# Performance work log

Hardware: AMD Instinct MI355X
Metric: run time of the kernel (lower is better)

The kernel has to match this reference:

```python
import jax, jax.numpy as jnp
import numpy as np

B, N, M, D, H = 2, 4096, 4096, 512, 8
P = D // H


def setup_inputs() -> dict:
    key = jax.random.key(0)
    ks = jax.random.split(key, 9)
    s = 1.0 / np.sqrt(D)
    return {
        "queries": jax.random.normal(ks[0], (B, N, D), dtype=jnp.float32),
        "keys": jax.random.normal(ks[1], (B, M, D), dtype=jnp.float32),
        "values": jax.random.normal(ks[2], (B, M, D), dtype=jnp.float32),
        "Wq": jax.random.normal(ks[3], (D, D), dtype=jnp.float32) * s,
        "bq": jax.random.normal(ks[4], (D,), dtype=jnp.float32) * s,
        "Wk": jax.random.normal(ks[5], (D, D), dtype=jnp.float32) * s,
        "bk": jax.random.normal(ks[6], (D,), dtype=jnp.float32) * s,
        "Wv": jax.random.normal(ks[7], (D, D), dtype=jnp.float32) * s,
        "bv": jax.random.normal(ks[8], (D,), dtype=jnp.float32) * s,
    }


def reference(queries, keys, values, Wq, bq, Wk, bk, Wv, bv):
    b, n, d = queries.shape
    m = keys.shape[1]
    h, p = H, D // H
    temperature = jnp.asarray(p, queries.dtype) ** 0.5
    # Linear projections (torch Linear: x @ W^T + b; here W stored as [in, out])
    q = (queries @ Wq + bq).reshape(b, n, h, p)
    k = (keys @ Wk + bk).reshape(b, m, h, p)
    v = (values @ Wv + bv).reshape(b, m, h, p)
    # scaled dot-product attention per head; scores [b, h, n, m]
    scores = jnp.einsum("bnhp,bmhp->bhnm", q, k) / temperature
    attn = jax.nn.softmax(scores, axis=-1)
    out = jnp.einsum("bhnm,bmhp->bnhp", attn, v)
    return out.reshape(b, n, d)
```

## Files before the change

kernel.cpp:

```cpp
#include <hip/hip_runtime.h>
#include <stdint.h>

#define B_ 2
#define N_ 4096
#define M_ 4096
#define D_ 512
#define H_ 8
#define P_ 64

typedef short bf16x8 __attribute__((ext_vector_type(8)));
typedef float f32x4 __attribute__((ext_vector_type(4)));
typedef unsigned short u16;
typedef unsigned int u32;
typedef u32 u32x4 __attribute__((ext_vector_type(4)));

static __device__ __forceinline__ u16 f2bf(float f) {
  u32 u = __builtin_bit_cast(u32, f);
  u32 r = u + 0x7fffu + ((u >> 16) & 1u);
  return (u16)(r >> 16);
}

static __device__ __forceinline__ u32 cvtpk(float lo, float hi_) {
  u32 d;
  asm("v_cvt_pk_bf16_f32 %0, %1, %2" : "=v"(d) : "v"(lo), "v"(hi_));
  return d;
}

static __device__ __forceinline__ float fexp2(float x) {
  float r;
  asm("v_exp_f32 %0, %1" : "=v"(r) : "v"(x));
  return r;
}

static __device__ __forceinline__ u32 permpk(const bf16x8& a0, const bf16x8& a1, int i) {
  u32x4 a0w = __builtin_bit_cast(u32x4, a0);
  u32x4 a1w = __builtin_bit_cast(u32x4, a1);
  int wd = i >> 1;
  u32 sel = (i & 1) ? 0x07060302u : 0x05040100u;
  return __builtin_amdgcn_perm(a1w[wd], a0w[wd], sel);
}

__global__ __launch_bounds__(256) void wt_kernel(const float* __restrict__ Wq,
                                                 const float* __restrict__ Wk,
                                                 const float* __restrict__ Wv,
                                                 u16* __restrict__ Wt) {
  __shared__ float tile[32][33];
  int z = blockIdx.z;
  const float* W = (z == 0) ? Wq : (z == 1) ? Wk : Wv;
  u16* out = Wt + (size_t)z * D_ * D_;
  int o0 = blockIdx.x * 32, d0 = blockIdx.y * 32;
  int tx = threadIdx.x, ty = threadIdx.y;
#pragma unroll
  for (int k = 0; k < 4; k++) tile[ty + k * 8][tx] = W[(size_t)(d0 + ty + k * 8) * D_ + o0 + tx];
  __syncthreads();
#pragma unroll
  for (int k = 0; k < 4; k++) out[(size_t)(o0 + ty + k * 8) * D_ + d0 + tx] = f2bf(tile[tx][ty + k * 8]);
}

__global__ __launch_bounds__(256) void proj_kernel(const float* __restrict__ Xq,
                                                   const float* __restrict__ Xk,
                                                   const float* __restrict__ Xv,
                                                   const u16* __restrict__ Wt,
                                                   const float* __restrict__ bq,
                                                   const float* __restrict__ bk,
                                                   const float* __restrict__ bv,
                                                   u16* __restrict__ QKV) {
  int bid = blockIdx.x;
  int xcd = bid & 7, idx = bid >> 3;
  int xb = idx & 3, gg = idx >> 2;
  int yz = xcd + 8 * gg;
  int yb = yz & 63, z = yz >> 6;

  const float* X = (z == 0) ? Xq : (z == 1) ? Xk : Xv;
  const float* bias = (z == 0) ? bq : (z == 1) ? bk : bv;
  const u16* W = Wt + (size_t)z * D_ * D_;
  u16* Y = QKV + (size_t)z * (B_ * N_ * D_);
  const float scale = (z == 0) ? 0.18033688011112042f : 1.0f;

  __shared__ u16 Alds[2][128 * 32];
  __shared__ u16 Blds[2][128 * 32];
  char* AL = (char*)&Alds[0][0];
  char* BL = (char*)&Blds[0][0];

  int t = threadIdx.x;
  int lane = t & 63, w = t >> 6;
  int wm = w >> 1, wn = w & 1;
  int l15 = lane & 15, g = lane >> 4;
  int rb = yb * 128, ob = xb * 128;

  int awoff = (t >> 3) * 64 + (((t & 7) * 8) ^ (((t >> 3) & 3) << 4));
  int bwoff = (t >> 2) * 64 + (((t & 3) * 16) ^ (((t >> 2) & 3) << 4));
  const float* xg = X + (size_t)(rb + (t >> 3)) * D_ + (t & 7) * 4;
  const u16* wg = W + (size_t)(ob + (t >> 2)) * D_ + (t & 3) * 8;

  int aroff = (wm * 64 + l15) * 64 + ((g * 16) ^ ((l15 & 3) << 4));
  int broff = (wn * 64 + l15) * 64 + ((g * 16) ^ ((l15 & 3) << 4));

  const f32x4 zero4 = {0.f, 0.f, 0.f, 0.f};
  f32x4 acc[4][4];
#pragma unroll
  for (int m = 0; m < 4; m++)
#pragma unroll
    for (int n = 0; n < 4; n++) acc[m][n] = zero4;

  {
#pragma unroll
    for (int i = 0; i < 4; i++) {
      float4 v = *(const float4*)(xg + (size_t)(32 * i) * D_);
      uint2 d;
      d.x = cvtpk(v.x, v.y);
      d.y = cvtpk(v.z, v.w);
      *(uint2*)(AL + awoff + i * 2048) = d;
    }
#pragma unroll
    for (int i = 0; i < 2; i++)
      *(bf16x8*)(BL + bwoff + i * 4096) = *(const bf16x8*)(wg + (size_t)(64 * i) * D_);
  }
  awoff ^= 0x2000;
  bwoff ^= 0x2000;
  __syncthreads();

  for (int kt = 0; kt < 16; kt++) {
    float4 ax0 = {}, ax1 = {}, ax2 = {}, ax3 = {};
    bf16x8 bx0 = {}, bx1 = {};
    if (kt < 15) {
      const float* xp = xg + (kt + 1) * 32;
      const u16* wp = wg + (kt + 1) * 32;
      ax0 = *(const float4*)(xp);
      ax1 = *(const float4*)(xp + (size_t)32 * D_);
      ax2 = *(const float4*)(xp + (size_t)64 * D_);
      ax3 = *(const float4*)(xp + (size_t)96 * D_);
      bx0 = *(const bf16x8*)(wp);
      bx1 = *(const bf16x8*)(wp + (size_t)64 * D_);
    }

    bf16x8 a[4], b[4];
#pragma unroll
    for (int m = 0; m < 4; m++) a[m] = *(const bf16x8*)(AL + aroff + m * 1024);
#pragma unroll
    for (int n = 0; n < 4; n++) b[n] = *(const bf16x8*)(BL + broff + n * 1024);
#pragma unroll
    for (int m = 0; m < 4; m++)
#pragma unroll
      for (int n = 0; n < 4; n++)
        acc[m][n] = __builtin_amdgcn_mfma_f32_16x16x32_bf16(a[m], b[n], acc[m][n], 0, 0, 0);

    if (kt < 15) {
      uint2 d;
      d.x = cvtpk(ax0.x, ax0.y);
      d.y = cvtpk(ax0.z, ax0.w);
      *(uint2*)(AL + awoff) = d;
      d.x = cvtpk(ax1.x, ax1.y);
      d.y = cvtpk(ax1.z, ax1.w);
      *(uint2*)(AL + awoff + 2048) = d;
      d.x = cvtpk(ax2.x, ax2.y);
      d.y = cvtpk(ax2.z, ax2.w);
      *(uint2*)(AL + awoff + 4096) = d;
      d.x = cvtpk(ax3.x, ax3.y);
      d.y = cvtpk(ax3.z, ax3.w);
      *(uint2*)(AL + awoff + 6144) = d;
      *(bf16x8*)(BL + bwoff) = bx0;
      *(bf16x8*)(BL + bwoff + 4096) = bx1;
    }
    awoff ^= 0x2000;
    bwoff ^= 0x2000;
    aroff ^= 0x2000;
    broff ^= 0x2000;
    __syncthreads();
  }

#pragma unroll
  for (int n = 0; n < 4; n++) {
    int col = ob + wn * 64 + n * 16 + l15;
    float bv_ = bias[col];
#pragma unroll
    for (int m = 0; m < 4; m++) {
      int row0 = rb + wm * 64 + m * 16 + g * 4;
#pragma unroll
      for (int r = 0; r < 4; r++) {
        float y = (acc[m][n][r] + bv_) * scale;
        Y[(size_t)(row0 + r) * D_ + col] = f2bf(y);
      }
    }
  }
}

__global__ __launch_bounds__(512, 2) void attn_kernel(const u16* __restrict__ QKV,
                                                      float* __restrict__ out) {
  const u16* Q = QKV;
  const u16* K = QKV + (size_t)(B_ * N_ * D_);
  const u16* V = K + (size_t)(B_ * N_ * D_);

  __shared__ u16 Klds[2][128 * 64];
  __shared__ u16 Vlds[2][2][64 * 64];

  char* KL = (char*)&Klds[0][0];
  char* VL = (char*)&Vlds[0][0][0];

  int t = threadIdx.x, l = t & 63, w = t >> 6;
  int l15 = l & 15, g = (l >> 4) & 3;
  int swz = (l15 & 7) << 4;

  int bid = blockIdx.x + 16 * (blockIdx.y + 8 * blockIdx.z);
  int sbid = (bid & 7) * 32 + (bid >> 3);
  int qt = sbid & 15, h = (sbid >> 4) & 7, b = sbid >> 7;
  int qwa = qt * 256 + w * 16;
  int qwb = qwa + 128;

  const u16* Kb = K + (size_t)(b * M_) * D_ + h * P_;
  const u16* Vb = V + (size_t)(b * M_) * D_ + h * P_;

  bf16x8 qfa[2], qfb[2];
  const u16* qrow_a = Q + (size_t)(b * N_ + qwa + l15) * D_ + h * P_;
  const u16* qrow_b = Q + (size_t)(b * N_ + qwb + l15) * D_ + h * P_;
#pragma unroll
  for (int step = 0; step < 2; step++) {
    qfa[step] = *(const bf16x8*)(qrow_a + step * 32 + g * 8);
    qfb[step] = *(const bf16x8*)(qrow_b + step * 32 + g * 8);
  }

  int koff0 = l15 * 128 + ((g * 16) ^ swz);
  int koff1 = l15 * 128 + ((64 + g * 16) ^ swz);
  int voff0 = koff0, voff1 = koff1;

  int krow = t >> 3, kc = t & 7;
  int kwoff = krow * 128 + ((kc * 16) ^ ((krow & 7) << 4));
  const u16* kg0 = Kb + (size_t)krow * D_ + kc * 8;
  const u16* kg1 = kg0 + (size_t)64 * D_;
  int hv = t >> 8, th = t & 255;
  int kp = th & 31, p0 = (th >> 5) * 8;
  int kv0 = 2 * kp, blk2 = kv0 >> 5, ww_ = kv0 & 31;
  int slot = blk2 * 32 + ((ww_ >> 2) & 3) * 8 + ((ww_ >> 4) << 2) + (ww_ & 3);
  int vwB = hv * 0x2000 + p0 * 128 + 2 * slot;
  const u16* vg0 = Vb + (size_t)(hv * 64 + kv0) * D_ + p0;
  const u16* vg1 = vg0 + D_;

  const f32x4 zc = {0.f, 0.f, 0.f, 0.f};
  const u32x4 onesw = {0x3F803F80u, 0x3F803F80u, 0x3F803F80u, 0x3F803F80u};
  const bf16x8 ones_f = __builtin_bit_cast(bf16x8, onesw);
  f32x4 oa[4], ob_[4], ol_a = zc, ol_b = zc;
#pragma unroll
  for (int i = 0; i < 4; i++) {
    oa[i] = zc;
    ob_[i] = zc;
  }

  {
    *(bf16x8*)(KL + kwoff) = *(const bf16x8*)kg0;
    *(bf16x8*)(KL + kwoff + 8192) = *(const bf16x8*)kg1;
    bf16x8 a0 = *(const bf16x8*)vg0;
    bf16x8 a1 = *(const bf16x8*)vg1;
#pragma unroll
    for (int i = 0; i < 8; i++) *(u32*)(VL + ((vwB ^ (i << 4)) + i * 128)) = permpk(a0, a1, i);
  }
  kwoff ^= 0x4000;
  vwB ^= 0x4000;
  const u16* kgp0 = kg0 + (size_t)128 * D_;
  const u16* kgp1 = kg1 + (size_t)128 * D_;
  const u16* vgp0 = vg0 + (size_t)128 * D_;
  const u16* vgp1 = vg1 + (size_t)128 * D_;
  __syncthreads();

  const int NT = M_ / 128;
  for (int kt = 0; kt < NT; kt++) {
    bf16x8 kn0 = {}, kn1 = {}, vn0 = {}, vn1 = {};
    if (kt + 1 < NT) {
      kn0 = *(const bf16x8*)kgp0;
      kn1 = *(const bf16x8*)kgp1;
      vn0 = *(const bf16x8*)vgp0;
      vn1 = *(const bf16x8*)vgp1;
      kgp0 += (size_t)128 * D_;
      kgp1 += (size_t)128 * D_;
      vgp0 += (size_t)128 * D_;
      vgp1 += (size_t)128 * D_;
    }

    f32x4 sa0[4], sb0[4], sa1[4], sb1[4];

    __builtin_amdgcn_s_setprio(1);
#pragma unroll
    for (int tt = 0; tt < 4; tt++) {
      bf16x8 kf0 = *(const bf16x8*)(KL + koff0 + tt * 2048);
      sa0[tt] = __builtin_amdgcn_mfma_f32_16x16x32_bf16(kf0, qfa[0], zc, 0, 0, 0);
      sb0[tt] = __builtin_amdgcn_mfma_f32_16x16x32_bf16(kf0, qfb[0], zc, 0, 0, 0);
      bf16x8 kf1 = *(const bf16x8*)(KL + koff1 + tt * 2048);
      sa0[tt] = __builtin_amdgcn_mfma_f32_16x16x32_bf16(kf1, qfa[1], sa0[tt], 0, 0, 0);
      sb0[tt] = __builtin_amdgcn_mfma_f32_16x16x32_bf16(kf1, qfb[1], sb0[tt], 0, 0, 0);
    }
#pragma unroll
    for (int tt = 0; tt < 4; tt++) {
      bf16x8 kf0 = *(const bf16x8*)(KL + koff0 + 8192 + tt * 2048);
      sa1[tt] = __builtin_amdgcn_mfma_f32_16x16x32_bf16(kf0, qfa[0], zc, 0, 0, 0);
      sb1[tt] = __builtin_amdgcn_mfma_f32_16x16x32_bf16(kf0, qfb[0], zc, 0, 0, 0);
      bf16x8 kf1 = *(const bf16x8*)(KL + koff1 + 8192 + tt * 2048);
      sa1[tt] = __builtin_amdgcn_mfma_f32_16x16x32_bf16(kf1, qfa[1], sa1[tt], 0, 0, 0);
      sb1[tt] = __builtin_amdgcn_mfma_f32_16x16x32_bf16(kf1, qfb[1], sb1[tt], 0, 0, 0);
    }
    __builtin_amdgcn_s_setprio(0);

    u32 pwa0[2][4], pwb0[2][4];
#pragma unroll
    for (int tt = 0; tt < 4; tt++)
#pragma unroll
      for (int r = 0; r < 4; r++) {
        sa0[tt][r] = fexp2(sa0[tt][r]);
        sb0[tt][r] = fexp2(sb0[tt][r]);
      }
#pragma unroll
    for (int kb2 = 0; kb2 < 2; kb2++)
#pragma unroll
      for (int wd = 0; wd < 4; wd++) {
        const f32x4& sva = sa0[2 * kb2 + (wd >> 1)];
        const f32x4& svb = sb0[2 * kb2 + (wd >> 1)];
        pwa0[kb2][wd] = cvtpk(sva[(wd & 1) * 2], sva[(wd & 1) * 2 + 1]);
        pwb0[kb2][wd] = cvtpk(svb[(wd & 1) * 2], svb[(wd & 1) * 2 + 1]);
      }

    __builtin_amdgcn_s_setprio(1);
#pragma unroll
    for (int kb2 = 0; kb2 < 2; kb2++) {
      u32x4 pva = {pwa0[kb2][0], pwa0[kb2][1], pwa0[kb2][2], pwa0[kb2][3]};
      u32x4 pvb = {pwb0[kb2][0], pwb0[kb2][1], pwb0[kb2][2], pwb0[kb2][3]};
      bf16x8 pfa = __builtin_bit_cast(bf16x8, pva);
      bf16x8 pfb = __builtin_bit_cast(bf16x8, pvb);
      int voff = kb2 ? voff1 : voff0;
#pragma unroll
      for (int tt = 0; tt < 4; tt++) {
        bf16x8 vf = *(const bf16x8*)(VL + voff + tt * 2048);
        oa[tt] = __builtin_amdgcn_mfma_f32_16x16x32_bf16(vf, pfa, oa[tt], 0, 0, 0);
        ob_[tt] = __builtin_amdgcn_mfma_f32_16x16x32_bf16(vf, pfb, ob_[tt], 0, 0, 0);
      }
      ol_a = __builtin_amdgcn_mfma_f32_16x16x32_bf16(ones_f, pfa, ol_a, 0, 0, 0);
      ol_b = __builtin_amdgcn_mfma_f32_16x16x32_bf16(ones_f, pfb, ol_b, 0, 0, 0);
    }
    __builtin_amdgcn_s_setprio(0);

    u32 pwa1[2][4], pwb1[2][4];
#pragma unroll
    for (int tt = 0; tt < 4; tt++)
#pragma unroll
      for (int r = 0; r < 4; r++) {
        sa1[tt][r] = fexp2(sa1[tt][r]);
        sb1[tt][r] = fexp2(sb1[tt][r]);
      }
#pragma unroll
    for (int kb2 = 0; kb2 < 2; kb2++)
#pragma unroll
      for (int wd = 0; wd < 4; wd++) {
        const f32x4& sva = sa1[2 * kb2 + (wd >> 1)];
        const f32x4& svb = sb1[2 * kb2 + (wd >> 1)];
        pwa1[kb2][wd] = cvtpk(sva[(wd & 1) * 2], sva[(wd & 1) * 2 + 1]);
        pwb1[kb2][wd] = cvtpk(svb[(wd & 1) * 2], svb[(wd & 1) * 2 + 1]);
      }

    __builtin_amdgcn_s_setprio(1);
#pragma unroll
    for (int kb2 = 0; kb2 < 2; kb2++) {
      u32x4 pva = {pwa1[kb2][0], pwa1[kb2][1], pwa1[kb2][2], pwa1[kb2][3]};
      u32x4 pvb = {pwb1[kb2][0], pwb1[kb2][1], pwb1[kb2][2], pwb1[kb2][3]};
      bf16x8 pfa = __builtin_bit_cast(bf16x8, pva);
      bf16x8 pfb = __builtin_bit_cast(bf16x8, pvb);
      int voff = (kb2 ? voff1 : voff0) + 0x2000;
#pragma unroll
      for (int tt = 0; tt < 4; tt++) {
        bf16x8 vf = *(const bf16x8*)(VL + voff + tt * 2048);
        oa[tt] = __builtin_amdgcn_mfma_f32_16x16x32_bf16(vf, pfa, oa[tt], 0, 0, 0);
        ob_[tt] = __builtin_amdgcn_mfma_f32_16x16x32_bf16(vf, pfb, ob_[tt], 0, 0, 0);
      }
      ol_a = __builtin_amdgcn_mfma_f32_16x16x32_bf16(ones_f, pfa, ol_a, 0, 0, 0);
      ol_b = __builtin_amdgcn_mfma_f32_16x16x32_bf16(ones_f, pfb, ol_b, 0, 0, 0);
    }
    __builtin_amdgcn_s_setprio(0);

    if (kt + 1 < NT) {
      *(bf16x8*)(KL + kwoff) = kn0;
      *(bf16x8*)(KL + kwoff + 8192) = kn1;
#pragma unroll
      for (int i = 0; i < 8; i++) *(u32*)(VL + ((vwB ^ (i << 4)) + i * 128)) = permpk(vn0, vn1, i);
    }
    koff0 ^= 0x4000;
    koff1 ^= 0x4000;
    voff0 ^= 0x4000;
    voff1 ^= 0x4000;
    kwoff ^= 0x4000;
    vwB ^= 0x4000;
    __syncthreads();
  }

  float rla = 1.0f / ol_a[0], rlb = 1.0f / ol_b[0];
  float* orow_a = out + (size_t)(b * N_ + qwa + l15) * D_ + h * P_;
  float* orow_b = out + (size_t)(b * N_ + qwb + l15) * D_ + h * P_;
#pragma unroll
  for (int tt = 0; tt < 4; tt++) {
    float4 sta = {oa[tt][0] * rla, oa[tt][1] * rla, oa[tt][2] * rla, oa[tt][3] * rla};
    *(float4*)(orow_a + tt * 16 + g * 4) = sta;
    float4 stb = {ob_[tt][0] * rlb, ob_[tt][1] * rlb, ob_[tt][2] * rlb, ob_[tt][3] * rlb};
    *(float4*)(orow_b + tt * 16 + g * 4) = stb;
  }
}

extern "C" void kernel_launch(void* const* d_in, const int* in_sizes, int n_in,
                              void* d_out, int out_size, void* d_ws, size_t ws_size,
                              hipStream_t stream) {
  const float* queries = (const float*)d_in[0];
  const float* keys = (const float*)d_in[1];
  const float* values = (const float*)d_in[2];
  const float* Wq = (const float*)d_in[3];
  const float* bq = (const float*)d_in[4];
  const float* Wk = (const float*)d_in[5];
  const float* bk = (const float*)d_in[6];
  const float* Wv = (const float*)d_in[7];
  const float* bv = (const float*)d_in[8];
  float* out = (float*)d_out;

  u16* QKV = (u16*)d_ws;
  u16* Wt = QKV + (size_t)3 * B_ * N_ * D_;

  wt_kernel<<<dim3(16, 16, 3), dim3(32, 8), 0, stream>>>(Wq, Wk, Wv, Wt);
  proj_kernel<<<768, 256, 0, stream>>>(queries, keys, values, Wt, bq, bk, bv, QKV);
  attn_kernel<<<dim3(16, 8, 2), 512, 0, stream>>>(QKV, out);
}
```

Measured before the change: 107.4 us.

## Software-pipeline attention by deferring second-half softmax/PV across iterations

Restructures the attention main loop into a 4-way unrolled pipeline. The second half of each K tile's scores is carried into the next iteration, where its exp/convert/PV work overlaps the next tile's QK MFMAs. V staging is split into a double-buffered first half and a 4-deep ring for the deferred second half, with a drain step after the loop. The launch bound drops from two blocks per CU to one, freeing registers for the extra live score tiles at the cost of occupancy.

Result: faster. 105.3 us (-2.0%).

```diff
diff --git a/kernel.cpp b/kernel.cpp
--- a/kernel.cpp
+++ b/kernel.cpp
@@ -185,17 +185,164 @@
   }
 }
 
-__global__ __launch_bounds__(512, 2) void attn_kernel(const u16* __restrict__ QKV,
+struct AttnCtx {
+  const bf16x8* qfa;
+  const bf16x8* qfb;
+  f32x4 (*oa)[4];
+  f32x4 (*ob)[4];
+  f32x4* ol_a;
+  f32x4* ol_b;
+  char* KL;
+  char* V0L;
+  char* V1L;
+  int kro0, kro1, vro0, vro1, kwoff, vwloc, hv;
+  bf16x8 ones_f;
+};
+
+template <int U>
+static __device__ __forceinline__ void attn_pos(const AttnCtx& c, bool dodefer, bool dostage,
+                                                f32x4 (&cura)[4], f32x4 (&curb)[4],
+                                                f32x4 (&preva)[4], f32x4 (&prevb)[4],
+                                                const u16*& kgp0, const u16*& kgp1,
+                                                const u16*& vgp0, const u16*& vgp1) {
+  constexpr int KB = (U & 1) * 0x4000;
+  constexpr int V0B = (U & 1) * 0x2000;
+  constexpr int V1PREV = ((U + 3) & 3) * 0x2000;
+  constexpr int KBN = ((U + 1) & 1) * 0x4000;
+  constexpr int V0BN = ((U + 1) & 1) * 0x2000;
+  constexpr int V1BN = ((U + 1) & 3) * 0x2000;
+  const f32x4 zc = {0.f, 0.f, 0.f, 0.f};
+
+  bf16x8 kn0 = {}, kn1 = {}, vn0 = {}, vn1 = {};
+  if (dostage) {
+    kn0 = *(const bf16x8*)kgp0;
+    kn1 = *(const bf16x8*)kgp1;
+    vn0 = *(const bf16x8*)vgp0;
+    vn1 = *(const bf16x8*)vgp1;
+    kgp0 += (size_t)128 * D_;
+    kgp1 += (size_t)128 * D_;
+    vgp0 += (size_t)128 * D_;
+    vgp1 += (size_t)128 * D_;
+  }
+
+  f32x4 s0a[4], s0b[4];
+  __builtin_amdgcn_s_setprio(1);
+#pragma unroll
+  for (int tt = 0; tt < 4; tt++) {
+    bf16x8 kf0 = *(const bf16x8*)(c.KL + KB + c.kro0 + tt * 2048);
+    s0a[tt] = __builtin_amdgcn_mfma_f32_16x16x32_bf16(kf0, c.qfa[0], zc, 0, 0, 0);
+    s0b[tt] = __builtin_amdgcn_mfma_f32_16x16x32_bf16(kf0, c.qfb[0], zc, 0, 0, 0);
+    bf16x8 kf1 = *(const bf16x8*)(c.KL + KB + c.kro1 + tt * 2048);
+    s0a[tt] = __builtin_amdgcn_mfma_f32_16x16x32_bf16(kf1, c.qfa[1], s0a[tt], 0, 0, 0);
+    s0b[tt] = __builtin_amdgcn_mfma_f32_16x16x32_bf16(kf1, c.qfb[1], s0b[tt], 0, 0, 0);
+  }
+#pragma unroll
+  for (int tt = 0; tt < 4; tt++) {
+    bf16x8 kf0 = *(const bf16x8*)(c.KL + KB + 8192 + c.kro0 + tt * 2048);
+    cura[tt] = __builtin_amdgcn_mfma_f32_16x16x32_bf16(kf0, c.qfa[0], zc, 0, 0, 0);
+    curb[tt] = __builtin_amdgcn_mfma_f32_16x16x32_bf16(kf0, c.qfb[0], zc, 0, 0, 0);
+    bf16x8 kf1 = *(const bf16x8*)(c.KL + KB + 8192 + c.kro1 + tt * 2048);
+    cura[tt] = __builtin_amdgcn_mfma_f32_16x16x32_bf16(kf1, c.qfa[1], cura[tt], 0, 0, 0);
+    curb[tt] = __builtin_amdgcn_mfma_f32_16x16x32_bf16(kf1, c.qfb[1], curb[tt], 0, 0, 0);
+  }
+  __builtin_amdgcn_s_setprio(0);
+
+  if (dodefer) {
+    u32 pwa[2][4], pwb[2][4];
+#pragma unroll
+    for (int tt = 0; tt < 4; tt++)
+#pragma unroll
+      for (int r = 0; r < 4; r++) {
+        preva[tt][r] = fexp2(preva[tt][r]);
+        prevb[tt][r] = fexp2(prevb[tt][r]);
+      }
+#pragma unroll
+    for (int kb2 = 0; kb2 < 2; kb2++)
+#pragma unroll
+      for (int wd = 0; wd < 4; wd++) {
+        const f32x4& sva = preva[2 * kb2 + (wd >> 1)];
+        const f32x4& svb = prevb[2 * kb2 + (wd >> 1)];
+        pwa[kb2][wd] = cvtpk(sva[(wd & 1) * 2], sva[(wd & 1) * 2 + 1]);
+        pwb[kb2][wd] = cvtpk(svb[(wd & 1) * 2], svb[(wd & 1) * 2 + 1]);
+      }
+    __builtin_amdgcn_s_setprio(1);
+#pragma unroll
+    for (int kb2 = 0; kb2 < 2; kb2++) {
+      u32x4 pva = {pwa[kb2][0], pwa[kb2][1], pwa[kb2][2], pwa[kb2][3]};
+      u32x4 pvb = {pwb[kb2][0], pwb[kb2][1], pwb[kb2][2], pwb[kb2][3]};
+      bf16x8 pfa = __builtin_bit_cast(bf16x8, pva);
+      bf16x8 pfb = __builtin_bit_cast(bf16x8, pvb);
+      int voff = V1PREV + (kb2 ? c.vro1 : c.vro0);
+#pragma unroll
+      for (int tt = 0; tt < 4; tt++) {
+        bf16x8 vf = *(const bf16x8*)(c.V1L + voff + tt * 2048);
+        (*c.oa)[tt] = __builtin_amdgcn_mfma_f32_16x16x32_bf16(vf, pfa, (*c.oa)[tt], 0, 0, 0);
+        (*c.ob)[tt] = __builtin_amdgcn_mfma_f32_16x16x32_bf16(vf, pfb, (*c.ob)[tt], 0, 0, 0);
+      }
+      *c.ol_a = __builtin_amdgcn_mfma_f32_16x16x32_bf16(c.ones_f, pfa, *c.ol_a, 0, 0, 0);
+      *c.ol_b = __builtin_amdgcn_mfma_f32_16x16x32_bf16(c.ones_f, pfb, *c.ol_b, 0, 0, 0);
+    }
+    __builtin_amdgcn_s_setprio(0);
+  }
+
+  {
+    u32 pwa[2][4], pwb[2][4];
+#pragma unroll
+    for (int tt = 0; tt < 4; tt++)
+#pragma unroll
+      for (int r = 0; r < 4; r++) {
+        s0a[tt][r] = fexp2(s0a[tt][r]);
+        s0b[tt][r] = fexp2(s0b[tt][r]);
+      }
+#pragma unroll
+    for (int kb2 = 0; kb2 < 2; kb2++)
+#pragma unroll
+      for (int wd = 0; wd < 4; wd++) {
+        const f32x4& sva = s0a[2 * kb2 + (wd >> 1)];
+        const f32x4& svb = s0b[2 * kb2 + (wd >> 1)];
+        pwa[kb2][wd] = cvtpk(sva[(wd & 1) * 2], sva[(wd & 1) * 2 + 1]);
+        pwb[kb2][wd] = cvtpk(svb[(wd & 1) * 2], svb[(wd & 1) * 2 + 1]);
+      }
+    __builtin_amdgcn_s_setprio(1);
+#pragma unroll
+    for (int kb2 = 0; kb2 < 2; kb2++) {
+      u32x4 pva = {pwa[kb2][0], pwa[kb2][1], pwa[kb2][2], pwa[kb2][3]};
+      u32x4 pvb = {pwb[kb2][0], pwb[kb2][1], pwb[kb2][2], pwb[kb2][3]};
+      bf16x8 pfa = __builtin_bit_cast(bf16x8, pva);
+      bf16x8 pfb = __builtin_bit_cast(bf16x8, pvb);
+      int voff = V0B + (kb2 ? c.vro1 : c.vro0);
+#pragma unroll
+      for (int tt = 0; tt < 4; tt++) {
+        bf16x8 vf = *(const bf16x8*)(c.V0L + voff + tt * 2048);
+        (*c.oa)[tt] = __builtin_amdgcn_mfma_f32_16x16x32_bf16(vf, pfa, (*c.oa)[tt], 0, 0, 0);
+        (*c.ob)[tt] = __builtin_amdgcn_mfma_f32_16x16x32_bf16(vf, pfb, (*c.ob)[tt], 0, 0, 0);
+      }
+      *c.ol_a = __builtin_amdgcn_mfma_f32_16x16x32_bf16(c.ones_f, pfa, *c.ol_a, 0, 0, 0);
+      *c.ol_b = __builtin_amdgcn_mfma_f32_16x16x32_bf16(c.ones_f, pfb, *c.ol_b, 0, 0, 0);
+    }
+    __builtin_amdgcn_s_setprio(0);
+  }
+
+  if (dostage) {
+    *(bf16x8*)(c.KL + KBN + c.kwoff) = kn0;
+    *(bf16x8*)(c.KL + KBN + c.kwoff + 8192) = kn1;
+    char* vdst = c.hv ? (c.V1L + V1BN) : (c.V0L + V0BN);
+#pragma unroll
+    for (int i = 0; i < 8; i++)
+      *(u32*)(vdst + ((c.vwloc ^ (i << 4)) + i * 128)) = permpk(vn0, vn1, i);
+  }
+  __syncthreads();
+}
+
+__global__ __launch_bounds__(512, 1) void attn_kernel(const u16* __restrict__ QKV,
                                                       float* __restrict__ out) {
   const u16* Q = QKV;
   const u16* K = QKV + (size_t)(B_ * N_ * D_);
   const u16* V = K + (size_t)(B_ * N_ * D_);
 
   __shared__ u16 Klds[2][128 * 64];
-  __shared__ u16 Vlds[2][2][64 * 64];
-
-  char* KL = (char*)&Klds[0][0];
-  char* VL = (char*)&Vlds[0][0][0];
+  __shared__ u16 V0lds[2][64 * 64];
+  __shared__ u16 V1lds[4][64 * 64];
 
   int t = threadIdx.x, l = t & 63, w = t >> 6;
   int l15 = l & 15, g = (l >> 4) & 3;
@@ -219,172 +366,110 @@
     qfb[step] = *(const bf16x8*)(qrow_b + step * 32 + g * 8);
   }
 
-  int koff0 = l15 * 128 + ((g * 16) ^ swz);
-  int koff1 = l15 * 128 + ((64 + g * 16) ^ swz);
-  int voff0 = koff0, voff1 = koff1;
+  AttnCtx c;
+  c.qfa = qfa;
+  c.qfb = qfb;
+  c.KL = (char*)&Klds[0][0];
+  c.V0L = (char*)&V0lds[0][0];
+  c.V1L = (char*)&V1lds[0][0];
+  c.kro0 = l15 * 128 + ((g * 16) ^ swz);
+  c.kro1 = l15 * 128 + ((64 + g * 16) ^ swz);
+  c.vro0 = c.kro0;
+  c.vro1 = c.kro1;
 
   int krow = t >> 3, kc = t & 7;
-  int kwoff = krow * 128 + ((kc * 16) ^ ((krow & 7) << 4));
+  c.kwoff = krow * 128 + ((kc * 16) ^ ((krow & 7) << 4));
   const u16* kg0 = Kb + (size_t)krow * D_ + kc * 8;
   const u16* kg1 = kg0 + (size_t)64 * D_;
   int hv = t >> 8, th = t & 255;
+  c.hv = hv;
   int kp = th & 31, p0 = (th >> 5) * 8;
   int kv0 = 2 * kp, blk2 = kv0 >> 5, ww_ = kv0 & 31;
   int slot = blk2 * 32 + ((ww_ >> 2) & 3) * 8 + ((ww_ >> 4) << 2) + (ww_ & 3);
-  int vwB = hv * 0x2000 + p0 * 128 + 2 * slot;
+  c.vwloc = p0 * 128 + 2 * slot;
   const u16* vg0 = Vb + (size_t)(hv * 64 + kv0) * D_ + p0;
   const u16* vg1 = vg0 + D_;
 
   const f32x4 zc = {0.f, 0.f, 0.f, 0.f};
   const u32x4 onesw = {0x3F803F80u, 0x3F803F80u, 0x3F803F80u, 0x3F803F80u};
-  const bf16x8 ones_f = __builtin_bit_cast(bf16x8, onesw);
+  c.ones_f = __builtin_bit_cast(bf16x8, onesw);
   f32x4 oa[4], ob_[4], ol_a = zc, ol_b = zc;
 #pragma unroll
   for (int i = 0; i < 4; i++) {
     oa[i] = zc;
     ob_[i] = zc;
   }
+  c.oa = &oa;
+  c.ob = &ob_;
+  c.ol_a = &ol_a;
+  c.ol_b = &ol_b;
+
+  f32x4 sAa[4], sAb[4], sBa[4], sBb[4];
+#pragma unroll
+  for (int i = 0; i < 4; i++) {
+    sAa[i] = zc;
+    sAb[i] = zc;
+    sBa[i] = zc;
+    sBb[i] = zc;
+  }
 
   {
-    *(bf16x8*)(KL + kwoff) = *(const bf16x8*)kg0;
-    *(bf16x8*)(KL + kwoff + 8192) = *(const bf16x8*)kg1;
+    *(bf16x8*)(c.KL + c.kwoff) = *(const bf16x8*)kg0;
+    *(bf16x8*)(c.KL + c.kwoff + 8192) = *(const bf16x8*)kg1;
     bf16x8 a0 = *(const bf16x8*)vg0;
     bf16x8 a1 = *(const bf16x8*)vg1;
-#pragma unroll
-    for (int i = 0; i < 8; i++) *(u32*)(VL + ((vwB ^ (i << 4)) + i * 128)) = permpk(a0, a1, i);
-  }
-  kwoff ^= 0x4000;
-  vwB ^= 0x4000;
+    char* vdst = hv ? c.V1L : c.V0L;
+#pragma unroll
+    for (int i = 0; i < 8; i++)
+      *(u32*)(vdst + ((c.vwloc ^ (i << 4)) + i * 128)) = permpk(a0, a1, i);
+  }
   const u16* kgp0 = kg0 + (size_t)128 * D_;
   const u16* kgp1 = kg1 + (size_t)128 * D_;
   const u16* vgp0 = vg0 + (size_t)128 * D_;
   const u16* vgp1 = vg1 + (size_t)128 * D_;
   __syncthreads();
 
-  const int NT = M_ / 128;
-  for (int kt = 0; kt < NT; kt++) {
-    bf16x8 kn0 = {}, kn1 = {}, vn0 = {}, vn1 = {};
-    if (kt + 1 < NT) {
-      kn0 = *(const bf16x8*)kgp0;
-      kn1 = *(const bf16x8*)kgp1;
-      vn0 = *(const bf16x8*)vgp0;
-      vn1 = *(const bf16x8*)vgp1;
-      kgp0 += (size_t)128 * D_;
-      kgp1 += (size_t)128 * D_;
-      vgp0 += (size_t)128 * D_;
-      vgp1 += (size_t)128 * D_;
-    }
-
-    f32x4 sa0[4], sb0[4], sa1[4], sb1[4];
-
-    __builtin_amdgcn_s_setprio(1);
-#pragma unroll
-    for (int tt = 0; tt < 4; tt++) {
-      bf16x8 kf0 = *(const bf16x8*)(KL + koff0 + tt * 2048);
-      sa0[tt] = __builtin_amdgcn_mfma_f32_16x16x32_bf16(kf0, qfa[0], zc, 0, 0, 0);
-      sb0[tt] = __builtin_amdgcn_mfma_f32_16x16x32_bf16(kf0, qfb[0], zc, 0, 0, 0);
-      bf16x8 kf1 = *(const bf16x8*)(KL + koff1 + tt * 2048);
-      sa0[tt] = __builtin_amdgcn_mfma_f32_16x16x32_bf16(kf1, qfa[1], sa0[tt], 0, 0, 0);
-      sb0[tt] = __builtin_amdgcn_mfma_f32_16x16x32_bf16(kf1, qfb[1], sb0[tt], 0, 0, 0);
-    }
-#pragma unroll
-    for (int tt = 0; tt < 4; tt++) {
-      bf16x8 kf0 = *(const bf16x8*)(KL + koff0 + 8192 + tt * 2048);
-      sa1[tt] = __builtin_amdgcn_mfma_f32_16x16x32_bf16(kf0, qfa[0], zc, 0, 0, 0);
-      sb1[tt] = __builtin_amdgcn_mfma_f32_16x16x32_bf16(kf0, qfb[0], zc, 0, 0, 0);
-      bf16x8 kf1 = *(const bf16x8*)(KL + koff1 + 8192 + tt * 2048);
-      sa1[tt] = __builtin_amdgcn_mfma_f32_16x16x32_bf16(kf1, qfa[1], sa1[tt], 0, 0, 0);
-      sb1[tt] = __builtin_amdgcn_mfma_f32_16x16x32_bf16(kf1, qfb[1], sb1[tt], 0, 0, 0);
-    }
-    __builtin_amdgcn_s_setprio(0);
-
-    u32 pwa0[2][4], pwb0[2][4];
+  for (int j = 0; j < 8; j++) {
+    attn_pos<0>(c, j > 0, true, sAa, sAb, sBa, sBb, kgp0, kgp1, vgp0, vgp1);
+    attn_pos<1>(c, true, true, sBa, sBb, sAa, sAb, kgp0, kgp1, vgp0, vgp1);
+    attn_pos<2>(c, true, true, sAa, sAb, sBa, sBb, kgp0, kgp1, vgp0, vgp1);
+    attn_pos<3>(c, true, j < 7, sBa, sBb, sAa, sAb, kgp0, kgp1, vgp0, vgp1);
+  }
+
+  {
+    u32 pwa[2][4], pwb[2][4];
 #pragma unroll
     for (int tt = 0; tt < 4; tt++)
 #pragma unroll
       for (int r = 0; r < 4; r++) {
-        sa0[tt][r] = fexp2(sa0[tt][r]);
-        sb0[tt][r] = fexp2(sb0[tt][r]);
+        sBa[tt][r] = fexp2(sBa[tt][r]);
+        sBb[tt][r] = fexp2(sBb[tt][r]);
       }
 #pragma unroll
     for (int kb2 = 0; kb2 < 2; kb2++)
 #pragma unroll
       for (int wd = 0; wd < 4; wd++) {
-        const f32x4& sva = sa0[2 * kb2 + (wd >> 1)];
-        const f32x4& svb = sb0[2 * kb2 + (wd >> 1)];
-        pwa0[kb2][wd] = cvtpk(sva[(wd & 1) * 2], sva[(wd & 1) * 2 + 1]);
-        pwb0[kb2][wd] = cvtpk(svb[(wd & 1) * 2], svb[(wd & 1) * 2 + 1]);
-      }
-
-    __builtin_amdgcn_s_setprio(1);
+        const f32x4& sva = sBa[2 * kb2 + (wd >> 1)];
+        const f32x4& svb = sBb[2 * kb2 + (wd >> 1)];
+        pwa[kb2][wd] = cvtpk(sva[(wd & 1) * 2], sva[(wd & 1) * 2 + 1]);
+        pwb[kb2][wd] = cvtpk(svb[(wd & 1) * 2], svb[(wd & 1) * 2 + 1]);
+      }
 #pragma unroll
     for (int kb2 = 0; kb2 < 2; kb2++) {
-      u32x4 pva = {pwa0[kb2][0], pwa0[kb2][1], pwa0[kb2][2], pwa0[kb2][3]};
-      u32x4 pvb = {pwb0[kb2][0], pwb0[kb2][1], pwb0[kb2][2], pwb0[kb2][3]};
+      u32x4 pva = {pwa[kb2][0], pwa[kb2][1], pwa[kb2][2], pwa[kb2][3]};
+      u32x4 pvb = {pwb[kb2][0], pwb[kb2][1], pwb[kb2][2], pwb[kb2][3]};
       bf16x8 pfa = __builtin_bit_cast(bf16x8, pva);
       bf16x8 pfb = __builtin_bit_cast(bf16x8, pvb);
-      int voff = kb2 ? voff1 : voff0;
+      int voff = 3 * 0x2000 + (kb2 ? c.vro1 : c.vro0);
 #pragma unroll
       for (int tt = 0; tt < 4; tt++) {
-        bf16x8 vf = *(const bf16x8*)(VL + voff + tt * 2048);
+        bf16x8 vf = *(const bf16x8*)(c.V1L + voff + tt * 2048);
         oa[tt] = __builtin_amdgcn_mfma_f32_16x16x32_bf16(vf, pfa, oa[tt], 0, 0, 0);
         ob_[tt] = __builtin_amdgcn_mfma_f32_16x16x32_bf16(vf, pfb, ob_[tt], 0, 0, 0);
       }
-      ol_a = __builtin_amdgcn_mfma_f32_16x16x32_bf16(ones_f, pfa, ol_a, 0, 0, 0);
-      ol_b = __builtin_amdgcn_mfma_f32_16x16x32_bf16(ones_f, pfb, ol_b, 0, 0, 0);
-    }
-    __builtin_amdgcn_s_setprio(0);
-
-    u32 pwa1[2][4], pwb1[2][4];
-#pragma unroll
-    for (int tt = 0; tt < 4; tt++)
-#pragma unroll
-      for (int r = 0; r < 4; r++) {
-        sa1[tt][r] = fexp2(sa1[tt][r]);
-        sb1[tt][r] = fexp2(sb1[tt][r]);
-      }
-#pragma unroll
-    for (int kb2 = 0; kb2 < 2; kb2++)
-#pragma unroll
-      for (int wd = 0; wd < 4; wd++) {
-        const f32x4& sva = sa1[2 * kb2 + (wd >> 1)];
-        const f32x4& svb = sb1[2 * kb2 + (wd >> 1)];
-        pwa1[kb2][wd] = cvtpk(sva[(wd & 1) * 2], sva[(wd & 1) * 2 + 1]);
-        pwb1[kb2][wd] = cvtpk(svb[(wd & 1) * 2], svb[(wd & 1) * 2 + 1]);
-      }
-
-    __builtin_amdgcn_s_setprio(1);
-#pragma unroll
-    for (int kb2 = 0; kb2 < 2; kb2++) {
-      u32x4 pva = {pwa1[kb2][0], pwa1[kb2][1], pwa1[kb2][2], pwa1[kb2][3]};
-      u32x4 pvb = {pwb1[kb2][0], pwb1[kb2][1], pwb1[kb2][2], pwb1[kb2][3]};
-      bf16x8 pfa = __builtin_bit_cast(bf16x8, pva);
-      bf16x8 pfb = __builtin_bit_cast(bf16x8, pvb);
-      int voff = (kb2 ? voff1 : voff0) + 0x2000;
-#pragma unroll
-      for (int tt = 0; tt < 4; tt++) {
-        bf16x8 vf = *(const bf16x8*)(VL + voff + tt * 2048);
-        oa[tt] = __builtin_amdgcn_mfma_f32_16x16x32_bf16(vf, pfa, oa[tt], 0, 0, 0);
-        ob_[tt] = __builtin_amdgcn_mfma_f32_16x16x32_bf16(vf, pfb, ob_[tt], 0, 0, 0);
-      }
-      ol_a = __builtin_amdgcn_mfma_f32_16x16x32_bf16(ones_f, pfa, ol_a, 0, 0, 0);
-      ol_b = __builtin_amdgcn_mfma_f32_16x16x32_bf16(ones_f, pfb, ol_b, 0, 0, 0);
-    }
-    __builtin_amdgcn_s_setprio(0);
-
-    if (kt + 1 < NT) {
-      *(bf16x8*)(KL + kwoff) = kn0;
-      *(bf16x8*)(KL + kwoff + 8192) = kn1;
-#pragma unroll
-      for (int i = 0; i < 8; i++) *(u32*)(VL + ((vwB ^ (i << 4)) + i * 128)) = permpk(vn0, vn1, i);
-    }
-    koff0 ^= 0x4000;
-    koff1 ^= 0x4000;
-    voff0 ^= 0x4000;
-    voff1 ^= 0x4000;
-    kwoff ^= 0x4000;
-    vwB ^= 0x4000;
-    __syncthreads();
+      ol_a = __builtin_amdgcn_mfma_f32_16x16x32_bf16(c.ones_f, pfa, ol_a, 0, 0, 0);
+      ol_b = __builtin_amdgcn_mfma_f32_16x16x32_bf16(c.ones_f, pfb, ol_b, 0, 0, 0);
+    }
   }
 
   float rla = 1.0f / ol_a[0], rlb = 1.0f / ol_b[0];
```
